# Kernel tuning notes

Hardware: AMD Instinct MI355X
Metric: run time of the kernel (lower is better)

## Reference

```python
import jax, jax.numpy as jnp
import numpy as np

B, T, D, E, H, K = 4, 1024, 1024, 8, 4096, 2
N = B * T
EPS_LN = 1e-5
EPS_W = 1e-8
BAL_W = 0.01


def setup_inputs() -> dict:
    key = jax.random.key(0)
    ks = jax.random.split(key, 5)
    sc = 0.02
    return {
        "x": jax.random.normal(ks[0], (B, T, D), jnp.float32),
        "ln_gamma": jnp.ones((D,), jnp.float32),
        "ln_beta": jnp.zeros((D,), jnp.float32),
        "gate_w": jax.random.normal(ks[1], (D, E), jnp.float32) * sc,
        "w1": jax.random.normal(ks[2], (E, D, H), jnp.float32) * sc,
        "b1": jnp.zeros((E, H), jnp.float32),
        "w2": jax.random.normal(ks[3], (E, H, D), jnp.float32) * sc,
        "b2": jnp.zeros((E, D), jnp.float32),
    }


def reference(x, ln_gamma, ln_beta, gate_w, w1, b1, w2, b2):
    # LayerNorm (pre-norm), residual kept on raw x
    mu = jnp.mean(x, axis=-1, keepdims=True)
    var = jnp.var(x, axis=-1, keepdims=True)
    xn = (x - mu) * jax.lax.rsqrt(var + EPS_LN) * ln_gamma + ln_beta

    xf = xn.reshape(N, D)

    # Router (oscillator_state=None path): token gate only, k = top_k
    logits = xf @ gate_w                         # (N, E)
    router_probs = jax.nn.softmax(logits, axis=-1)
    top_w, top_i = jax.lax.top_k(router_probs, K)  # (N, K)
    top_w = top_w / (jnp.sum(top_w, axis=-1, keepdims=True) + EPS_W)

    # Dense per-token gate matrix: gates[n, e] = sum of top-k weights routed to e
    gates = jnp.zeros((N, E), xf.dtype).at[jnp.arange(N)[:, None], top_i].add(top_w)

    # Per-expert FFN (computed densely for all tokens, combined by sparse gates)
    h = jax.nn.gelu(jnp.einsum("nd,edh->enh", xf, w1) + b1[:, None, :], approximate=False)
    expert_out = jnp.einsum("enh,ehd->end", h, w2) + b2[:, None, :]  # (E, N, D)
    moe = jnp.einsum("ne,end->nd", gates, expert_out)

    output = x + moe.reshape(B, T, D)

    # Load-balance auxiliary loss
    counts = jnp.zeros((E,), xf.dtype).at[top_i.reshape(-1)].add(1.0)
    fraction = counts / N
    balance_loss = BAL_W * E * jnp.sum(fraction * jnp.mean(router_probs, axis=0))

    return output, balance_loss, router_probs
```

## Files before the change

kernel.cpp:

```cpp
#include <hip/hip_runtime.h>
#include <hip/hip_bf16.h>
#include <math.h>

#define DI   1024
#define EI   8
#define HI   4096
#define NI   4096

typedef __bf16 bf16x8 __attribute__((ext_vector_type(8)));
typedef float  f32x4  __attribute__((ext_vector_type(4)));

__device__ __forceinline__ unsigned short f2bf(float f) {
  union { float f; unsigned u; } c; c.f = f;
  unsigned r = c.u + 0x7FFF + ((c.u >> 16) & 1);
  return (unsigned short)(r >> 16);
}

__device__ __forceinline__ void async16(const void* g, void* l) {
  __builtin_amdgcn_global_load_lds(
      (const __attribute__((address_space(1))) void*)g,
      (__attribute__((address_space(3))) void*)l, 16, 0, 0);
}

__device__ __forceinline__ float gelu_fast(float v) {
  const float a = fabsf(v) * 0.70710678118f;
  const float t = __builtin_amdgcn_rcpf(fmaf(0.3275911f, a, 1.0f));
  float p = fmaf(1.061405429f, t, -1.453152027f);
  p = fmaf(p, t, 1.421413741f);
  p = fmaf(p, t, -0.284496736f);
  p = fmaf(p, t, 0.254829592f);
  p *= t;
  const float ex = __expf(-a * a);
  float er = fmaf(-p, ex, 1.0f);
  er = copysignf(er, v);
  return 0.5f * v * (1.0f + er);
}

#define MFMA_TILE(ASP, BSP)                                              \
  {                                                                      \
    _Pragma("unroll")                                                    \
    for (int kk = 0; kk < 2; kk++) {                                     \
      const int ko = ksw[kk];                                            \
      bf16x8 af[4], bfr[4];                                              \
      _Pragma("unroll")                                                  \
      for (int mi = 0; mi < 4; mi++)                                     \
        af[mi] = *(const bf16x8*)&(ASP)[(mrow + mi * 16) * 64 + ko];     \
      _Pragma("unroll")                                                  \
      for (int ni = 0; ni < 4; ni++)                                     \
        bfr[ni] = *(const bf16x8*)&(BSP)[(nrow + ni * 16) * 64 + ko];    \
      _Pragma("unroll")                                                  \
      for (int mi = 0; mi < 4; mi++)                                     \
        _Pragma("unroll")                                                \
        for (int ni = 0; ni < 4; ni++)                                   \
          acc[mi][ni] = __builtin_amdgcn_mfma_f32_16x16x32_bf16(         \
              af[mi], bfr[ni], acc[mi][ni], 0, 0, 0);                    \
    }                                                                    \
  }

__global__ __launch_bounds__(256) void ln_router_k(
    const float* __restrict__ x, const float* __restrict__ gamma,
    const float* __restrict__ beta, const float* __restrict__ gw,
    unsigned short* __restrict__ xnbf, float* __restrict__ probs_out,
    int* __restrict__ pairs, float2* __restrict__ gates2)
{
  const int t = threadIdx.x, lane = t & 63, wid = t >> 6;
  const int n = blockIdx.x * 4 + wid;

  const float4* xr = (const float4*)(x + (size_t)n * DI);
  float4 v[4];
  #pragma unroll
  for (int j = 0; j < 4; j++) v[j] = xr[lane * 4 + j];

  float s = 0.f, q = 0.f;
  #pragma unroll
  for (int j = 0; j < 4; j++) {
    s += v[j].x + v[j].y + v[j].z + v[j].w;
    q += v[j].x * v[j].x + v[j].y * v[j].y + v[j].z * v[j].z + v[j].w * v[j].w;
  }
  #pragma unroll
  for (int off = 1; off < 64; off <<= 1) {
    s += __shfl_xor(s, off);
    q += __shfl_xor(q, off);
  }
  const float mu = s * (1.0f / DI);
  const float rs = rsqrtf(q * (1.0f / DI) - mu * mu + 1e-5f);

  const float4* gr = (const float4*)gamma;
  const float4* br = (const float4*)beta;
  float xl[16];
  #pragma unroll
  for (int j = 0; j < 4; j++) {
    const float4 g4 = gr[lane * 4 + j];
    const float4 b4 = br[lane * 4 + j];
    xl[4 * j + 0] = (v[j].x - mu) * rs * g4.x + b4.x;
    xl[4 * j + 1] = (v[j].y - mu) * rs * g4.y + b4.y;
    xl[4 * j + 2] = (v[j].z - mu) * rs * g4.z + b4.z;
    xl[4 * j + 3] = (v[j].w - mu) * rs * g4.w + b4.w;
  }
  unsigned u[8];
  #pragma unroll
  for (int j = 0; j < 8; j++)
    u[j] = (unsigned)f2bf(xl[2 * j]) | ((unsigned)f2bf(xl[2 * j + 1]) << 16);
  uint4* dst = (uint4*)(xnbf + (size_t)n * DI + lane * 16);
  uint4 d0; d0.x = u[0]; d0.y = u[1]; d0.z = u[2]; d0.w = u[3];
  uint4 d1; d1.x = u[4]; d1.y = u[5]; d1.z = u[6]; d1.w = u[7];
  dst[0] = d0; dst[1] = d1;

  float p[8];
  #pragma unroll
  for (int e = 0; e < 8; e++) p[e] = 0.f;
  #pragma unroll
  for (int j = 0; j < 16; j++) {
    const float4* grow = (const float4*)(gw + (size_t)(lane * 16 + j) * EI);
    const float4 ga = grow[0], gb = grow[1];
    const float xv = xl[j];
    p[0] += xv * ga.x; p[1] += xv * ga.y; p[2] += xv * ga.z; p[3] += xv * ga.w;
    p[4] += xv * gb.x; p[5] += xv * gb.y; p[6] += xv * gb.z; p[7] += xv * gb.w;
  }
  #pragma unroll
  for (int e = 0; e < 8; e++)
    #pragma unroll
    for (int off = 1; off < 64; off <<= 1) p[e] += __shfl_xor(p[e], off);

  if (lane == 0) {
    float pm = -1e30f;
    #pragma unroll
    for (int e = 0; e < 8; e++) pm = fmaxf(pm, p[e]);
    float pr[8], ps = 0.f;
    #pragma unroll
    for (int e = 0; e < 8; e++) { pr[e] = expf(p[e] - pm); ps += pr[e]; }
    const float inv = 1.0f / ps;
    #pragma unroll
    for (int e = 0; e < 8; e++) {
      pr[e] *= inv;
      probs_out[(size_t)n * EI + e] = pr[e];
    }
    int i0 = 0; float m0 = pr[0];
    #pragma unroll
    for (int e = 1; e < 8; e++) if (pr[e] > m0) { m0 = pr[e]; i0 = e; }
    int i1 = -1; float m1 = -1e30f;
    #pragma unroll
    for (int e = 0; e < 8; e++) if (e != i0 && pr[e] > m1) { m1 = pr[e]; i1 = e; }
    const float ssum = m0 + m1 + 1e-8f;
    pairs[n] = i0 | (i1 << 8);
    float2 g2; g2.x = m0 / ssum; g2.y = m1 / ssum;
    gates2[n] = g2;
  }
}

__global__ __launch_bounds__(1024) void build_lists_k(
    const int* __restrict__ pairs, const float2* __restrict__ gates2,
    const float* __restrict__ probs, int* __restrict__ counts,
    int* __restrict__ offs, int* __restrict__ tok_list,
    float* __restrict__ gate_list, int2* __restrict__ ipos,
    float* __restrict__ out_bal)
{
  __shared__ int cnt[8];
  __shared__ int cur[8];
  __shared__ float wps[16][8];
  __shared__ float ps[8];
  const int t = threadIdx.x, lane = t & 63, wid = t >> 6;
  if (t < 8) cnt[t] = 0;
  __syncthreads();

  float acc[8];
  #pragma unroll
  for (int e = 0; e < 8; e++) acc[e] = 0.f;
  for (int n = t; n < NI; n += 1024) {
    const int pr = pairs[n];
    atomicAdd(&cnt[pr & 255], 1);
    atomicAdd(&cnt[pr >> 8], 1);
    const float4* prow = (const float4*)(probs + (size_t)n * EI);
    const float4 a = prow[0], b = prow[1];
    acc[0] += a.x; acc[1] += a.y; acc[2] += a.z; acc[3] += a.w;
    acc[4] += b.x; acc[5] += b.y; acc[6] += b.z; acc[7] += b.w;
  }
  #pragma unroll
  for (int e = 0; e < 8; e++)
    #pragma unroll
    for (int off = 1; off < 64; off <<= 1) acc[e] += __shfl_xor(acc[e], off);
  if (lane == 0)
    #pragma unroll
    for (int e = 0; e < 8; e++) wps[wid][e] = acc[e];
  __syncthreads();
  if (t < 8) {
    float sm = 0.f;
    for (int w = 0; w < 16; w++) sm += wps[w][t];
    ps[t] = sm;
  }
  __syncthreads();
  if (t == 0) {
    int off = 0; float bl = 0.f;
    for (int e = 0; e < 8; e++) {
      offs[e] = off; cur[e] = off; counts[e] = cnt[e];
      bl += (float)cnt[e] * ps[e];
      off += cnt[e];
    }
    *out_bal = 0.01f * 8.0f * bl / ((float)NI * (float)NI);
  }
  __syncthreads();
  for (int n = t; n < NI; n += 1024) {
    const int pr = pairs[n];
    const float2 g = gates2[n];
    const int p0 = atomicAdd(&cur[pr & 255], 1);
    tok_list[p0] = n; gate_list[p0] = g.x;
    const int p1 = atomicAdd(&cur[pr >> 8], 1);
    tok_list[p1] = n; gate_list[p1] = g.y;
    int2 ip; ip.x = p0; ip.y = p1;
    ipos[n] = ip;
  }
}

__global__ __launch_bounds__(256) void transpose_cvt_k(
    const float* __restrict__ in, unsigned short* __restrict__ out, int R, int C)
{
  __shared__ float tile[64][65];
  const size_t eoff = (size_t)blockIdx.z * (size_t)R * (size_t)C;
  const int c0 = blockIdx.x * 64, r0 = blockIdx.y * 64;
  const int t = threadIdx.x;
  {
    const int col = (t & 15) * 4;
    #pragma unroll
    for (int ii = 0; ii < 4; ii++) {
      const int row = (t >> 4) + ii * 16;
      const float4 v = *(const float4*)(in + eoff + (size_t)(r0 + row) * C + c0 + col);
      tile[row][col + 0] = v.x; tile[row][col + 1] = v.y;
      tile[row][col + 2] = v.z; tile[row][col + 3] = v.w;
    }
  }
  __syncthreads();
  {
    const int grp = t & 7;
    #pragma unroll
    for (int jj = 0; jj < 2; jj++) {
      const int orow = (t >> 3) + jj * 32;
      unsigned short vs[8];
      #pragma unroll
      for (int u = 0; u < 8; u++) vs[u] = f2bf(tile[grp * 8 + u][orow]);
      uint4 pk;
      pk.x = (unsigned)vs[0] | ((unsigned)vs[1] << 16);
      pk.y = (unsigned)vs[2] | ((unsigned)vs[3] << 16);
      pk.z = (unsigned)vs[4] | ((unsigned)vs[5] << 16);
      pk.w = (unsigned)vs[6] | ((unsigned)vs[7] << 16);
      *(uint4*)(out + eoff + (size_t)(c0 + orow) * R + r0 + grp * 8) = pk;
    }
  }
}

__global__ __launch_bounds__(256) void copy_x_k(const float* __restrict__ x, float* __restrict__ out)
{
  const size_t i = (size_t)blockIdx.x * 256 + threadIdx.x;
  ((float4*)out)[i] = ((const float4*)x)[i];
}

__global__ __launch_bounds__(256) void ffn1_k(
    const unsigned short* __restrict__ xnbf, const unsigned short* __restrict__ w1t,
    const float* __restrict__ b1, unsigned short* __restrict__ hbuf,
    const int* __restrict__ tok_list, const int* __restrict__ counts,
    const int* __restrict__ offsets)
{
  const int e = blockIdx.z;
  const int cnt = counts[e];
  const int mt = blockIdx.y;
  if (mt * 128 >= cnt) return;
  const int n0 = blockIdx.x * 128;
  const int t = threadIdx.x, lane = t & 63, w = t >> 6;
  const int wm = w & 1, wn = w >> 1;
  __shared__ __align__(16) unsigned short As[2][128 * 64];
  __shared__ __align__(16) unsigned short Bs[2][128 * 64];

  const int sub = lane >> 3;
  const int kc = (((lane & 7) ^ sub) * 8);
  const int eoff = offsets[e];
  const unsigned short* baseA[4];
  const unsigned short* baseB[4];
  #pragma unroll
  for (int r = 0; r < 4; r++) {
    int row = (w << 5) + r * 8 + sub;
    int idx = mt * 128 + row; if (idx > cnt - 1) idx = cnt - 1;
    int tok = tok_list[eoff + idx];
    baseA[r] = xnbf + (size_t)tok * DI + kc;
    baseB[r] = w1t + (size_t)e * HI * DI + (size_t)(n0 + row) * DI + kc;
  }

  f32x4 acc[4][4];
  const f32x4 zz = {0.f, 0.f, 0.f, 0.f};
  #pragma unroll
  for (int i = 0; i < 4; i++)
    #pragma unroll
    for (int j = 0; j < 4; j++) acc[i][j] = zz;

  const int mrow = (wm << 6) + (lane & 15);
  const int nrow = (wn << 6) + (lane & 15);
  const int ksw[2] = { (((lane >> 4) ^ (lane & 7)) * 8),
                       ((((lane >> 4) + 4) ^ (lane & 7)) * 8) };

  #pragma unroll
  for (int r = 0; r < 4; r++) {
    async16(baseA[r], &As[0][((w << 5) + r * 8) * 64]);
    async16(baseB[r], &Bs[0][((w << 5) + r * 8) * 64]);
  }
  __syncthreads();

  #pragma unroll 2
  for (int ti = 1; ti < DI / 64; ti++) {
    const int nb = ti & 1;
    const int cb = nb ^ 1;
    const int k0 = ti * 64;
    #pragma unroll
    for (int r = 0; r < 4; r++) {
      async16(baseA[r] + k0, &As[nb][((w << 5) + r * 8) * 64]);
      async16(baseB[r] + k0, &Bs[nb][((w << 5) + r * 8) * 64]);
    }
    MFMA_TILE(As[cb], Bs[cb]);
    __syncthreads();
  }
  MFMA_TILE(As[(DI / 64 - 1) & 1], Bs[(DI / 64 - 1) & 1]);

  const int hb = eoff + mt * 128;
  #pragma unroll
  for (int ni = 0; ni < 4; ni++) {
    const int col = n0 + (wn << 6) + ni * 16 + (lane & 15);
    const float bias = b1[e * HI + col];
    #pragma unroll
    for (int mi = 0; mi < 4; mi++) {
      #pragma unroll
      for (int rg = 0; rg < 4; rg++) {
        const int rowl = (wm << 6) + mi * 16 + ((lane >> 4) << 2) + rg;
        if (mt * 128 + rowl < cnt) {
          const float vv = gelu_fast(acc[mi][ni][rg] + bias);
          hbuf[(size_t)(hb + rowl) * HI + col] = f2bf(vv);
        }
      }
    }
  }
}

__global__ __launch_bounds__(256) void ffn2_k(
    const unsigned short* __restrict__ hbuf, const unsigned short* __restrict__ w2t,
    const float* __restrict__ b2, float* __restrict__ out,
    const int* __restrict__ tok_list, const float* __restrict__ gate_list,
    const int* __restrict__ counts, const int* __restrict__ offsets,
    float* __restrict__ eo)
{
  const int e = blockIdx.z;
  const int cnt = counts[e];
  const int mt = blockIdx.y;
  if (mt * 128 >= cnt) return;
  const int n0 = blockIdx.x * 128;
  const int t = threadIdx.x, lane = t & 63, w = t >> 6;
  const int wm = w & 1, wn = w >> 1;
  __shared__ __align__(16) unsigned short As[2][128 * 64];
  __shared__ __align__(16) unsigned short Bs[2][128 * 64];

  const int sub = lane >> 3;
  const int kc = (((lane & 7) ^ sub) * 8);
  const int eoff = offsets[e];
  const int hb = eoff + mt * 128;
  const unsigned short* baseA[4];
  const unsigned short* baseB[4];
  #pragma unroll
  for (int r = 0; r < 4; r++) {
    int row = (w << 5) + r * 8 + sub;
    baseA[r] = hbuf + (size_t)(hb + row) * HI + kc;
    baseB[r] = w2t + (size_t)e * DI * HI + (size_t)(n0 + row) * HI + kc;
  }

  f32x4 acc[4][4];
  const f32x4 zz = {0.f, 0.f, 0.f, 0.f};
  #pragma unroll
  for (int i = 0; i < 4; i++)
    #pragma unroll
    for (int j = 0; j < 4; j++) acc[i][j] = zz;

  const int mrow = (wm << 6) + (lane & 15);
  const int nrow = (wn << 6) + (lane & 15);
  const int ksw[2] = { (((lane >> 4) ^ (lane & 7)) * 8),
                       ((((lane >> 4) + 4) ^ (lane & 7)) * 8) };

  #pragma unroll
  for (int r = 0; r < 4; r++) {
    async16(baseA[r], &As[0][((w << 5) + r * 8) * 64]);
    async16(baseB[r], &Bs[0][((w << 5) + r * 8) * 64]);
  }
  __syncthreads();

  #pragma unroll 2
  for (int ti = 1; ti < HI / 64; ti++) {
    const int nb = ti & 1;
    const int cb = nb ^ 1;
    const int k0 = ti * 64;
    #pragma unroll
    for (int r = 0; r < 4; r++) {
      async16(baseA[r] + k0, &As[nb][((w << 5) + r * 8) * 64]);
      async16(baseB[r] + k0, &Bs[nb][((w << 5) + r * 8) * 64]);
    }
    MFMA_TILE(As[cb], Bs[cb]);
    __syncthreads();
  }
  MFMA_TILE(As[(HI / 64 - 1) & 1], Bs[(HI / 64 - 1) & 1]);

  float bias[4];
  #pragma unroll
  for (int ni = 0; ni < 4; ni++)
    bias[ni] = b2[e * DI + n0 + (wn << 6) + ni * 16 + (lane & 15)];

  if (eo) {
    #pragma unroll
    for (int mi = 0; mi < 4; mi++) {
      #pragma unroll
      for (int rg = 0; rg < 4; rg++) {
        const int rowl = (wm << 6) + mi * 16 + ((lane >> 4) << 2) + rg;
        const int gidx = mt * 128 + rowl;
        if (gidx < cnt) {
          float* erow = eo + (size_t)(hb + rowl) * DI;
          #pragma unroll
          for (int ni = 0; ni < 4; ni++) {
            const int col = n0 + (wn << 6) + ni * 16 + (lane & 15);
            erow[col] = acc[mi][ni][rg] + bias[ni];
          }
        }
      }
    }
  } else {
    #pragma unroll
    for (int mi = 0; mi < 4; mi++) {
      #pragma unroll
      for (int rg = 0; rg < 4; rg++) {
        const int rowl = (wm << 6) + mi * 16 + ((lane >> 4) << 2) + rg;
        const int gidx = mt * 128 + rowl;
        if (gidx < cnt) {
          const int tok = tok_list[eoff + gidx];
          const float gte = gate_list[eoff + gidx];
          float* orow = out + (size_t)tok * DI;
          #pragma unroll
          for (int ni = 0; ni < 4; ni++) {
            const int col = n0 + (wn << 6) + ni * 16 + (lane & 15);
            atomicAdd(orow + col, (acc[mi][ni][rg] + bias[ni]) * gte);
          }
        }
      }
    }
  }
}

__global__ __launch_bounds__(256) void combine_k(
    const float* __restrict__ x, const float* __restrict__ eo,
    const int2* __restrict__ ipos, const float2* __restrict__ gates2,
    float* __restrict__ out)
{
  const int n = blockIdx.x, t = threadIdx.x;
  const int2 pp = ipos[n];
  const float2 gg = gates2[n];
  const float4 a = ((const float4*)(x  + (size_t)n    * DI))[t];
  const float4 b = ((const float4*)(eo + (size_t)pp.x * DI))[t];
  const float4 c = ((const float4*)(eo + (size_t)pp.y * DI))[t];
  float4 r;
  r.x = a.x + gg.x * b.x + gg.y * c.x;
  r.y = a.y + gg.x * b.y + gg.y * c.y;
  r.z = a.z + gg.x * b.z + gg.y * c.z;
  r.w = a.w + gg.x * b.w + gg.y * c.w;
  ((float4*)(out + (size_t)n * DI))[t] = r;
}

extern "C" void kernel_launch(void* const* d_in, const int* in_sizes, int n_in,
                              void* d_out, int out_size, void* d_ws, size_t ws_size,
                              hipStream_t stream)
{
  const float* x   = (const float*)d_in[0];
  const float* gam = (const float*)d_in[1];
  const float* bet = (const float*)d_in[2];
  const float* gw  = (const float*)d_in[3];
  const float* w1  = (const float*)d_in[4];
  const float* b1  = (const float*)d_in[5];
  const float* w2  = (const float*)d_in[6];
  const float* b2  = (const float*)d_in[7];
  float* out = (float*)d_out;

  char* ws = (char*)d_ws;
  int*    counts = (int*)(ws + 0);
  int*    offs   = (int*)(ws + 64);
  int*    pairs  = (int*)(ws + 1024);
  float2* gates2 = (float2*)(ws + 20480);
  int*    tok    = (int*)(ws + 57344);
  float*  gate   = (float*)(ws + 90112);
  int2*   ipos   = (int2*)(ws + 122880);
  unsigned short* xnbf = (unsigned short*)(ws + 262656);
  unsigned short* wt   = (unsigned short*)(ws + 8651264);
  unsigned short* hbuf = (unsigned short*)(ws + 75760128);
  const bool use_eo = (ws_size >= 177472000ull);
  float* eo = use_eo ? (float*)(ws + 143917568) : (float*)nullptr;

  float* bal_out   = out + (size_t)NI * DI;
  float* probs_out = bal_out + 1;

  ln_router_k<<<NI / 4, 256, 0, stream>>>(x, gam, bet, gw, xnbf, probs_out, pairs, gates2);
  build_lists_k<<<1, 1024, 0, stream>>>(pairs, gates2, probs_out, counts, offs, tok, gate, ipos, bal_out);
  transpose_cvt_k<<<dim3(HI / 64, DI / 64, EI), 256, 0, stream>>>(w1, wt, DI, HI);
  if (!use_eo)
    copy_x_k<<<(NI * DI / 4) / 256, 256, 0, stream>>>(x, out);
  ffn1_k<<<dim3(HI / 128, NI / 128, EI), 256, 0, stream>>>(xnbf, wt, b1, hbuf, tok, counts, offs);
  transpose_cvt_k<<<dim3(DI / 64, HI / 64, EI), 256, 0, stream>>>(w2, wt, HI, DI);
  ffn2_k<<<dim3(DI / 128, NI / 128, EI), 256, 0, stream>>>(hbuf, wt, b2, out, tok, gate, counts, offs, eo);
  if (use_eo)
    combine_k<<<NI, 256, 0, stream>>>(x, eo, ipos, gates2, out);
}
```

Baseline: 675.1 us.

## Enlarge ffn1 tiles to 256x256 and rework ffn2 scheduling and buffering

ffn1 moves from a 128x128 tile with 256 threads to a 256x256 tile with 512 threads (8 waves). This doubles operand reuse per LDS load and halves the number of blocks. Its K-loop now syncs with raw s_barrier and explicit vmcnt/lgkmcnt waits instead of __syncthreads. ffn2 remaps its block index so consecutive blocks share a weight column tile, and drops double buffering for a single LDS buffer with two barriers per K step. That last change gives up load/compute overlap in ffn2, and ffn1's larger LDS footprint and register use limits how many blocks fit per CU.

```diff
diff --git a/kernel.cpp b/kernel.cpp
--- a/kernel.cpp
+++ b/kernel.cpp
@@ -36,7 +36,7 @@
   return 0.5f * v * (1.0f + er);
 }
 
-#define MFMA_TILE(ASP, BSP)                                              \
+#define MFMA_TILE_128(ASP, BSP)                                          \
   {                                                                      \
     _Pragma("unroll")                                                    \
     for (int kk = 0; kk < 2; kk++) {                                     \
@@ -253,7 +253,7 @@
   ((float4*)out)[i] = ((const float4*)x)[i];
 }
 
-__global__ __launch_bounds__(256) void ffn1_k(
+__global__ __launch_bounds__(512, 2) void ffn1_k(
     const unsigned short* __restrict__ xnbf, const unsigned short* __restrict__ w1t,
     const float* __restrict__ b1, unsigned short* __restrict__ hbuf,
     const int* __restrict__ tok_list, const int* __restrict__ counts,
@@ -262,72 +262,112 @@
   const int e = blockIdx.z;
   const int cnt = counts[e];
   const int mt = blockIdx.y;
-  if (mt * 128 >= cnt) return;
-  const int n0 = blockIdx.x * 128;
+  if (mt * 256 >= cnt) return;
+  const int n0 = blockIdx.x * 256;
   const int t = threadIdx.x, lane = t & 63, w = t >> 6;
   const int wm = w & 1, wn = w >> 1;
-  __shared__ __align__(16) unsigned short As[2][128 * 64];
-  __shared__ __align__(16) unsigned short Bs[2][128 * 64];
+  __shared__ __align__(16) unsigned short As[2][256 * 64];
+  __shared__ __align__(16) unsigned short Bs[2][256 * 64];
 
   const int sub = lane >> 3;
-  const int kc = (((lane & 7) ^ sub) * 8);
+  const int kc  = (((lane & 7) ^ sub) * 8);
   const int eoff = offsets[e];
   const unsigned short* baseA[4];
   const unsigned short* baseB[4];
   #pragma unroll
   for (int r = 0; r < 4; r++) {
-    int row = (w << 5) + r * 8 + sub;
-    int idx = mt * 128 + row; if (idx > cnt - 1) idx = cnt - 1;
-    int tok = tok_list[eoff + idx];
+    const int row = w * 32 + r * 8 + sub;
+    int idx = mt * 256 + row; if (idx > cnt - 1) idx = cnt - 1;
+    const int tok = tok_list[eoff + idx];
     baseA[r] = xnbf + (size_t)tok * DI + kc;
     baseB[r] = w1t + (size_t)e * HI * DI + (size_t)(n0 + row) * DI + kc;
   }
 
-  f32x4 acc[4][4];
+  f32x4 acc[8][4];
   const f32x4 zz = {0.f, 0.f, 0.f, 0.f};
   #pragma unroll
-  for (int i = 0; i < 4; i++)
+  for (int i = 0; i < 8; i++)
     #pragma unroll
     for (int j = 0; j < 4; j++) acc[i][j] = zz;
 
-  const int mrow = (wm << 6) + (lane & 15);
-  const int nrow = (wn << 6) + (lane & 15);
+  const int mrow = wm * 128 + (lane & 15);
+  const int nrow = wn * 64 + (lane & 15);
   const int ksw[2] = { (((lane >> 4) ^ (lane & 7)) * 8),
                        ((((lane >> 4) + 4) ^ (lane & 7)) * 8) };
 
   #pragma unroll
   for (int r = 0; r < 4; r++) {
-    async16(baseA[r], &As[0][((w << 5) + r * 8) * 64]);
-    async16(baseB[r], &Bs[0][((w << 5) + r * 8) * 64]);
-  }
-  __syncthreads();
-
+    async16(baseA[r], &As[0][(w * 32 + r * 8) * 64]);
+    async16(baseB[r], &Bs[0][(w * 32 + r * 8) * 64]);
+  }
+
+  const int NT = DI / 64;
   #pragma unroll 2
-  for (int ti = 1; ti < DI / 64; ti++) {
-    const int nb = ti & 1;
-    const int cb = nb ^ 1;
-    const int k0 = ti * 64;
+  for (int ti = 0; ti < NT - 1; ++ti) {
+    const int cur = ti & 1, nxt = cur ^ 1;
+    __builtin_amdgcn_s_barrier();
+    const int k0 = (ti + 1) * 64;
     #pragma unroll
     for (int r = 0; r < 4; r++) {
-      async16(baseA[r] + k0, &As[nb][((w << 5) + r * 8) * 64]);
-      async16(baseB[r] + k0, &Bs[nb][((w << 5) + r * 8) * 64]);
-    }
-    MFMA_TILE(As[cb], Bs[cb]);
-    __syncthreads();
-  }
-  MFMA_TILE(As[(DI / 64 - 1) & 1], Bs[(DI / 64 - 1) & 1]);
-
-  const int hb = eoff + mt * 128;
+      async16(baseA[r] + k0, &As[nxt][(w * 32 + r * 8) * 64]);
+      async16(baseB[r] + k0, &Bs[nxt][(w * 32 + r * 8) * 64]);
+    }
+    asm volatile("s_waitcnt vmcnt(8)" ::: "memory");
+    __builtin_amdgcn_s_barrier();
+    #pragma unroll
+    for (int kk = 0; kk < 2; kk++) {
+      const int ko = ksw[kk];
+      bf16x8 af[8], bfr[4];
+      #pragma unroll
+      for (int ni = 0; ni < 4; ni++)
+        bfr[ni] = *(const bf16x8*)&Bs[cur][(nrow + ni * 16) * 64 + ko];
+      #pragma unroll
+      for (int mi = 0; mi < 8; mi++)
+        af[mi] = *(const bf16x8*)&As[cur][(mrow + mi * 16) * 64 + ko];
+      #pragma unroll
+      for (int mi = 0; mi < 8; mi++)
+        #pragma unroll
+        for (int ni = 0; ni < 4; ni++)
+          acc[mi][ni] = __builtin_amdgcn_mfma_f32_16x16x32_bf16(
+              af[mi], bfr[ni], acc[mi][ni], 0, 0, 0);
+    }
+    asm volatile("s_waitcnt lgkmcnt(0)" ::: "memory");
+  }
+  __builtin_amdgcn_s_barrier();
+  asm volatile("s_waitcnt vmcnt(0)" ::: "memory");
+  __builtin_amdgcn_s_barrier();
+  {
+    const int cur = (NT - 1) & 1;
+    #pragma unroll
+    for (int kk = 0; kk < 2; kk++) {
+      const int ko = ksw[kk];
+      bf16x8 af[8], bfr[4];
+      #pragma unroll
+      for (int ni = 0; ni < 4; ni++)
+        bfr[ni] = *(const bf16x8*)&Bs[cur][(nrow + ni * 16) * 64 + ko];
+      #pragma unroll
+      for (int mi = 0; mi < 8; mi++)
+        af[mi] = *(const bf16x8*)&As[cur][(mrow + mi * 16) * 64 + ko];
+      #pragma unroll
+      for (int mi = 0; mi < 8; mi++)
+        #pragma unroll
+        for (int ni = 0; ni < 4; ni++)
+          acc[mi][ni] = __builtin_amdgcn_mfma_f32_16x16x32_bf16(
+              af[mi], bfr[ni], acc[mi][ni], 0, 0, 0);
+    }
+  }
+
+  const int hb = eoff + mt * 256;
   #pragma unroll
   for (int ni = 0; ni < 4; ni++) {
-    const int col = n0 + (wn << 6) + ni * 16 + (lane & 15);
+    const int col = n0 + wn * 64 + ni * 16 + (lane & 15);
     const float bias = b1[e * HI + col];
     #pragma unroll
-    for (int mi = 0; mi < 4; mi++) {
+    for (int mi = 0; mi < 8; mi++) {
       #pragma unroll
       for (int rg = 0; rg < 4; rg++) {
-        const int rowl = (wm << 6) + mi * 16 + ((lane >> 4) << 2) + rg;
-        if (mt * 128 + rowl < cnt) {
+        const int rowl = wm * 128 + mi * 16 + ((lane >> 4) << 2) + rg;
+        if (mt * 256 + rowl < cnt) {
           const float vv = gelu_fast(acc[mi][ni][rg] + bias);
           hbuf[(size_t)(hb + rowl) * HI + col] = f2bf(vv);
         }
@@ -343,15 +383,17 @@
     const int* __restrict__ counts, const int* __restrict__ offsets,
     float* __restrict__ eo)
 {
-  const int e = blockIdx.z;
+  const int r  = blockIdx.x + 8 * blockIdx.y;
+  const int e  = blockIdx.z;
+  const int nx = r >> 5;
+  const int mt = r & 31;
   const int cnt = counts[e];
-  const int mt = blockIdx.y;
   if (mt * 128 >= cnt) return;
-  const int n0 = blockIdx.x * 128;
+  const int n0 = nx * 128;
   const int t = threadIdx.x, lane = t & 63, w = t >> 6;
   const int wm = w & 1, wn = w >> 1;
-  __shared__ __align__(16) unsigned short As[2][128 * 64];
-  __shared__ __align__(16) unsigned short Bs[2][128 * 64];
+  __shared__ __align__(16) unsigned short As[128 * 64];
+  __shared__ __align__(16) unsigned short Bs[128 * 64];
 
   const int sub = lane >> 3;
   const int kc = (((lane & 7) ^ sub) * 8);
@@ -360,10 +402,10 @@
   const unsigned short* baseA[4];
   const unsigned short* baseB[4];
   #pragma unroll
-  for (int r = 0; r < 4; r++) {
-    int row = (w << 5) + r * 8 + sub;
-    baseA[r] = hbuf + (size_t)(hb + row) * HI + kc;
-    baseB[r] = w2t + (size_t)e * DI * HI + (size_t)(n0 + row) * HI + kc;
+  for (int rr = 0; rr < 4; rr++) {
+    const int row = (w << 5) + rr * 8 + sub;
+    baseA[rr] = hbuf + (size_t)(hb + row) * HI + kc;
+    baseB[rr] = w2t + (size_t)e * DI * HI + (size_t)(n0 + row) * HI + kc;
   }
 
   f32x4 acc[4][4];
@@ -378,27 +420,16 @@
   const int ksw[2] = { (((lane >> 4) ^ (lane & 7)) * 8),
                        ((((lane >> 4) + 4) ^ (lane & 7)) * 8) };
 
-  #pragma unroll
-  for (int r = 0; r < 4; r++) {
-    async16(baseA[r], &As[0][((w << 5) + r * 8) * 64]);
-    async16(baseB[r], &Bs[0][((w << 5) + r * 8) * 64]);
-  }
-  __syncthreads();
-
-  #pragma unroll 2
-  for (int ti = 1; ti < HI / 64; ti++) {
-    const int nb = ti & 1;
-    const int cb = nb ^ 1;
-    const int k0 = ti * 64;
-    #pragma unroll
-    for (int r = 0; r < 4; r++) {
-      async16(baseA[r] + k0, &As[nb][((w << 5) + r * 8) * 64]);
-      async16(baseB[r] + k0, &Bs[nb][((w << 5) + r * 8) * 64]);
-    }
-    MFMA_TILE(As[cb], Bs[cb]);
+  for (int k0 = 0; k0 < HI; k0 += 64) {
     __syncthreads();
-  }
-  MFMA_TILE(As[(HI / 64 - 1) & 1], Bs[(HI / 64 - 1) & 1]);
+    #pragma unroll
+    for (int rr = 0; rr < 4; rr++) {
+      async16(baseA[rr] + k0, &As[((w << 5) + rr * 8) * 64]);
+      async16(baseB[rr] + k0, &Bs[((w << 5) + rr * 8) * 64]);
+    }
+    __syncthreads();
+    MFMA_TILE_128(As, Bs);
+  }
 
   float bias[4];
   #pragma unroll
@@ -499,7 +530,7 @@
   transpose_cvt_k<<<dim3(HI / 64, DI / 64, EI), 256, 0, stream>>>(w1, wt, DI, HI);
   if (!use_eo)
     copy_x_k<<<(NI * DI / 4) / 256, 256, 0, stream>>>(x, out);
-  ffn1_k<<<dim3(HI / 128, NI / 128, EI), 256, 0, stream>>>(xnbf, wt, b1, hbuf, tok, counts, offs);
+  ffn1_k<<<dim3(HI / 256, 16, EI), 512, 0, stream>>>(xnbf, wt, b1, hbuf, tok, counts, offs);
   transpose_cvt_k<<<dim3(DI / 64, HI / 64, EI), 256, 0, stream>>>(w2, wt, HI, DI);
   ffn2_k<<<dim3(DI / 128, NI / 128, EI), 256, 0, stream>>>(hbuf, wt, b2, out, tok, gate, counts, offs, eo);
   if (use_eo)
```

After: 794.6 us. 1.18x slower.

## Single-buffer ffn1 LDS and rework ffn2 pipeline with 32-wide K tiles

Applied to the files above, without the earlier changes.

ffn1 drops LDS double buffering and uses a simple load/sync/compute loop over 64-wide K tiles, halving its shared memory to raise occupancy. ffn2 switches to 32-wide K tiles with a new XOR swizzle, keeps double buffering, and uses explicit vmcnt waits and raw barriers so the next tile's async loads overlap with the current MFMAs. The trade-off is loss of load/compute overlap in ffn1 and twice as many barrier iterations in ffn2. Partial waitcnt handling and the new swizzle add correctness risk.

```diff
diff --git a/kernel.cpp b/kernel.cpp
--- a/kernel.cpp
+++ b/kernel.cpp
@@ -36,7 +36,7 @@
   return 0.5f * v * (1.0f + er);
 }
 
-#define MFMA_TILE(ASP, BSP)                                              \
+#define MFMA_TILE_128(ASP, BSP)                                          \
   {                                                                      \
     _Pragma("unroll")                                                    \
     for (int kk = 0; kk < 2; kk++) {                                     \
@@ -266,8 +266,8 @@
   const int n0 = blockIdx.x * 128;
   const int t = threadIdx.x, lane = t & 63, w = t >> 6;
   const int wm = w & 1, wn = w >> 1;
-  __shared__ __align__(16) unsigned short As[2][128 * 64];
-  __shared__ __align__(16) unsigned short Bs[2][128 * 64];
+  __shared__ __align__(16) unsigned short As[128 * 64];
+  __shared__ __align__(16) unsigned short Bs[128 * 64];
 
   const int sub = lane >> 3;
   const int kc = (((lane & 7) ^ sub) * 8);
@@ -295,27 +295,16 @@
   const int ksw[2] = { (((lane >> 4) ^ (lane & 7)) * 8),
                        ((((lane >> 4) + 4) ^ (lane & 7)) * 8) };
 
-  #pragma unroll
-  for (int r = 0; r < 4; r++) {
-    async16(baseA[r], &As[0][((w << 5) + r * 8) * 64]);
-    async16(baseB[r], &Bs[0][((w << 5) + r * 8) * 64]);
-  }
-  __syncthreads();
-
-  #pragma unroll 2
-  for (int ti = 1; ti < DI / 64; ti++) {
-    const int nb = ti & 1;
-    const int cb = nb ^ 1;
-    const int k0 = ti * 64;
+  for (int k0 = 0; k0 < DI; k0 += 64) {
+    __syncthreads();
     #pragma unroll
     for (int r = 0; r < 4; r++) {
-      async16(baseA[r] + k0, &As[nb][((w << 5) + r * 8) * 64]);
-      async16(baseB[r] + k0, &Bs[nb][((w << 5) + r * 8) * 64]);
-    }
-    MFMA_TILE(As[cb], Bs[cb]);
+      async16(baseA[r] + k0, &As[((w << 5) + r * 8) * 64]);
+      async16(baseB[r] + k0, &Bs[((w << 5) + r * 8) * 64]);
+    }
     __syncthreads();
-  }
-  MFMA_TILE(As[(DI / 64 - 1) & 1], Bs[(DI / 64 - 1) & 1]);
+    MFMA_TILE_128(As, Bs);
+  }
 
   const int hb = eoff + mt * 128;
   #pragma unroll
@@ -350,20 +339,19 @@
   const int n0 = blockIdx.x * 128;
   const int t = threadIdx.x, lane = t & 63, w = t >> 6;
   const int wm = w & 1, wn = w >> 1;
-  __shared__ __align__(16) unsigned short As[2][128 * 64];
-  __shared__ __align__(16) unsigned short Bs[2][128 * 64];
-
-  const int sub = lane >> 3;
-  const int kc = (((lane & 7) ^ sub) * 8);
+  __shared__ __align__(16) unsigned short As[2][128 * 32];
+  __shared__ __align__(16) unsigned short Bs[2][128 * 32];
+
+  const int kc = (((lane & 3) ^ ((lane >> 3) & 3)) * 8);
   const int eoff = offsets[e];
   const int hb = eoff + mt * 128;
-  const unsigned short* baseA[4];
-  const unsigned short* baseB[4];
-  #pragma unroll
-  for (int r = 0; r < 4; r++) {
-    int row = (w << 5) + r * 8 + sub;
-    baseA[r] = hbuf + (size_t)(hb + row) * HI + kc;
-    baseB[r] = w2t + (size_t)e * DI * HI + (size_t)(n0 + row) * HI + kc;
+  const unsigned short* baseA[2];
+  const unsigned short* baseB[2];
+  #pragma unroll
+  for (int is = 0; is < 2; is++) {
+    const int row = w * 32 + is * 16 + (lane >> 2);
+    baseA[is] = hbuf + (size_t)(hb + row) * HI + kc;
+    baseB[is] = w2t + (size_t)e * DI * HI + (size_t)(n0 + row) * HI + kc;
   }
 
   f32x4 acc[4][4];
@@ -375,30 +363,52 @@
 
   const int mrow = (wm << 6) + (lane & 15);
   const int nrow = (wn << 6) + (lane & 15);
-  const int ksw[2] = { (((lane >> 4) ^ (lane & 7)) * 8),
-                       ((((lane >> 4) + 4) ^ (lane & 7)) * 8) };
-
-  #pragma unroll
-  for (int r = 0; r < 4; r++) {
-    async16(baseA[r], &As[0][((w << 5) + r * 8) * 64]);
-    async16(baseB[r], &Bs[0][((w << 5) + r * 8) * 64]);
-  }
-  __syncthreads();
-
-  #pragma unroll 2
-  for (int ti = 1; ti < HI / 64; ti++) {
-    const int nb = ti & 1;
-    const int cb = nb ^ 1;
-    const int k0 = ti * 64;
-    #pragma unroll
-    for (int r = 0; r < 4; r++) {
-      async16(baseA[r] + k0, &As[nb][((w << 5) + r * 8) * 64]);
-      async16(baseB[r] + k0, &Bs[nb][((w << 5) + r * 8) * 64]);
-    }
-    MFMA_TILE(As[cb], Bs[cb]);
-    __syncthreads();
-  }
-  MFMA_TILE(As[(HI / 64 - 1) & 1], Bs[(HI / 64 - 1) & 1]);
+  const int ko = ((lane >> 4) ^ (((lane & 15) >> 1) & 3)) * 8;
+
+  #define STAGE2(buf, k0s)                                                    \
+    {                                                                         \
+      _Pragma("unroll")                                                       \
+      for (int is = 0; is < 2; is++) {                                        \
+        async16(baseA[is] + (k0s), &As[buf][(w * 32 + is * 16) * 32]);        \
+        async16(baseB[is] + (k0s), &Bs[buf][(w * 32 + is * 16) * 32]);        \
+      }                                                                       \
+    }
+
+  #define MFMA_TILE_32(buf)                                                   \
+    {                                                                         \
+      bf16x8 af[4], bfr[4];                                                   \
+      _Pragma("unroll")                                                       \
+      for (int mi = 0; mi < 4; mi++)                                          \
+        af[mi] = *(const bf16x8*)&As[buf][(mrow + mi * 16) * 32 + ko];        \
+      _Pragma("unroll")                                                       \
+      for (int ni = 0; ni < 4; ni++)                                          \
+        bfr[ni] = *(const bf16x8*)&Bs[buf][(nrow + ni * 16) * 32 + ko];       \
+      _Pragma("unroll")                                                       \
+      for (int mi = 0; mi < 4; mi++)                                          \
+        _Pragma("unroll")                                                     \
+        for (int ni = 0; ni < 4; ni++)                                        \
+          acc[mi][ni] = __builtin_amdgcn_mfma_f32_16x16x32_bf16(              \
+              af[mi], bfr[ni], acc[mi][ni], 0, 0, 0);                         \
+    }
+
+  const int NT = HI / 32;
+  STAGE2(0, 0)
+
+  for (int ti = 0; ti < NT - 1; ++ti) {
+    const int cur = ti & 1, nxt = cur ^ 1;
+    STAGE2(nxt, (ti + 1) * 32)
+    asm volatile("s_waitcnt vmcnt(4)" ::: "memory");
+    __builtin_amdgcn_s_barrier();
+    MFMA_TILE_32(cur)
+    asm volatile("s_waitcnt lgkmcnt(0)" ::: "memory");
+    __builtin_amdgcn_s_barrier();
+  }
+  asm volatile("s_waitcnt vmcnt(0)" ::: "memory");
+  __builtin_amdgcn_s_barrier();
+  MFMA_TILE_32((NT - 1) & 1)
+
+  #undef STAGE2
+  #undef MFMA_TILE_32
 
   float bias[4];
   #pragma unroll
```

After: 648.5 us. -3.9%, faster.
